# Performance work log

Hardware: AMD Instinct MI355X
Metric: run time of the kernel (lower is better)

The kernel has to match this reference:

```python
import jax, jax.numpy as jnp
import numpy as np
from math import sqrt

S, B = 512, 64
V, E, H, T = 50000, 256, 512, 9
PAD = 0

def setup_inputs() -> dict:
    key = jax.random.key(0)
    ks = jax.random.split(key, 12)
    x = jax.random.randint(ks[0], (S, B), 0, V)
    x = x.at[0].set(jnp.maximum(x[0], 1))  # first token never pad (CRF mask req)
    bio = jax.random.randint(ks[1], (S, B), 0, T)
    sc = 0.02
    return {
        "x": x, "bio": bio,
        "emb": jax.random.normal(ks[2], (V, E), jnp.float32) * sc,
        "W_ih": jax.random.normal(ks[3], (4 * H, E), jnp.float32) * sc,
        "W_hh": jax.random.normal(ks[4], (4 * H, H), jnp.float32) * sc,
        "b_ih": jnp.zeros((4 * H,), jnp.float32),
        "b_hh": jnp.zeros((4 * H,), jnp.float32),
        "W_out": jax.random.normal(ks[5], (T, H), jnp.float32) * sc,
        "b_out": jnp.zeros((T,), jnp.float32),
        "start_t": jax.random.normal(ks[6], (T,), jnp.float32) * 0.1,
        "end_t": jax.random.normal(ks[7], (T,), jnp.float32) * 0.1,
        "trans": jax.random.normal(ks[8], (T, T), jnp.float32) * 0.1,
    }

def _lstm(embeds, W_ih, W_hh, b_ih, b_hh):
    # embeds: [S,B,E] time-major, single layer, pytorch gate order i,f,g,o
    def step(carry, e_t):
        h, c = carry
        gates = e_t @ W_ih.T + h @ W_hh.T + (b_ih + b_hh)  # [B,4H]
        i, f, g, o = jnp.split(gates, 4, axis=-1)
        i, f, o = jax.nn.sigmoid(i), jax.nn.sigmoid(f), jax.nn.sigmoid(o)
        c = f * c + i * jnp.tanh(g)
        h = o * jnp.tanh(c)
        return (h, c), h
    h0 = jnp.zeros((embeds.shape[1], W_hh.shape[1]), embeds.dtype)
    _, hs = jax.lax.scan(step, (h0, h0), embeds)
    return hs  # [S,B,H]

def _crf_llh(emissions, tags, maskf, start_t, end_t, trans):
    # emissions [S,B,T], tags [S,B], maskf [S,B] float. Returns summed log-likelihood.
    Bn = emissions.shape[1]
    barange = jnp.arange(Bn)
    em = jnp.take_along_axis(emissions, tags[:, :, None], axis=2)[:, :, 0]  # [S,B]
    tr = trans[tags[:-1], tags[1:]]  # [S-1,B]
    seq_ends = maskf.sum(0).astype(jnp.int32) - 1
    last_tags = tags[seq_ends, barange]
    num = (start_t[tags[0]] + em[0]
           + ((em[1:] + tr) * maskf[1:]).sum(0)
           + end_t[last_tags])  # [B]
    # normalizer: forward algorithm
    def step(score, inp):
        e_t, m_t = inp  # [B,T], [B]
        nxt = jax.nn.logsumexp(score[:, :, None] + trans[None] + e_t[:, None, :], axis=1)
        score = jnp.where(m_t[:, None] > 0, nxt, score)
        return score, None
    score0 = start_t[None] + emissions[0]  # [B,T]
    scoreN, _ = jax.lax.scan(step, score0, (emissions[1:], maskf[1:]))
    norm = jax.nn.logsumexp(scoreN + end_t[None], axis=1)  # [B]
    return (num - norm).sum()

def _viterbi(emissions, start_t, end_t, trans):
    # full-length decode (model calls crf.decode without mask)
    Bn, Tn = emissions.shape[1], emissions.shape[2]
    barange = jnp.arange(Bn)
    def step(score, e_t):
        cand = score[:, :, None] + trans[None]  # [B,T_prev,T_next]
        idx = jnp.argmax(cand, axis=1)          # [B,T]
        score = jnp.max(cand, axis=1) + e_t
        return score, idx
    score0 = start_t[None] + emissions[0]
    scoreN, history = jax.lax.scan(step, score0, emissions[1:])  # history [S-1,B,T]
    last = jnp.argmax(scoreN + end_t[None], axis=1)  # [B]
    def back(tag, h_t):
        prev = h_t[barange, tag]
        return prev, tag
    tag0, rest = jax.lax.scan(back, last, history, reverse=True)  # rest[t] = tag_{t+1}
    return jnp.concatenate([tag0[None], rest], axis=0)  # [S,B]

def reference(x, bio, emb, W_ih, W_hh, b_ih, b_hh, W_out, b_out, start_t, end_t, trans):
    maskf = (x != PAD).astype(jnp.float32)  # [S,B]
    embeds = emb[x] * sqrt(E)               # [S,B,E]
    lstm_out = _lstm(embeds, W_ih, W_hh, b_ih, b_hh)  # [S,B,H]
    logits = lstm_out @ W_out.T + b_out               # [S,B,T]
    emissions = jax.nn.log_softmax(logits, axis=-1)
    llh = _crf_llh(emissions, bio, maskf, start_t, end_t, trans)
    crf_tags = _viterbi(emissions, start_t, end_t, trans)
    return (-llh, crf_tags)
```

## Files before the change

### kernel.cpp

```cpp
#include <hip/hip_runtime.h>
#include <math.h>

#define SS 512
#define BB 64
#define EE 256
#define HH 512
#define NT 9
#define NWG 256
#define GBG 32

#define HS_ELEMS ((size_t)SS * BB * HH)
#define EM_OFF   HS_ELEMS
#define NUM_OFF  (EM_OFF + (size_t)SS * BB * NT)
#define NORM_OFF (NUM_OFF + 64)
#define BAR_OFF  (NORM_OFF + 64)
#define BAR_U32S ((size_t)SS * 8 * 16)

#define L_WHH 0
#define L_H   32768
#define L_GSM 36928
#define L_CS  37504
#define L_TOT 37632

__global__ __launch_bounds__(256) void init_barriers(float* __restrict__ ws) {
    unsigned* bar = (unsigned*)(ws + BAR_OFF);
    size_t idx = (size_t)blockIdx.x * 256 + threadIdx.x;
    if (idx < 2 * BAR_U32S) bar[idx] = 0u;
}

__global__ __launch_bounds__(512) void lstm_persistent(
    const float* __restrict__ Whh, const float* __restrict__ Wih,
    const float* __restrict__ bih, const float* __restrict__ bhh,
    const float* __restrict__ emb, const int* __restrict__ x,
    float* __restrict__ ws)
{
    const int wg    = blockIdx.x;
    const int slice = wg & 31;
    const int bg    = wg >> 5;
    const int tid   = threadIdx.x;
    const int w     = tid >> 6;
    const int L     = tid & 63;
    const int b_l   = L & 7;
    const int kc    = L >> 3;
    const int b     = bg * 8 + b_l;

    float* hs = ws;
    unsigned* cnt  = (unsigned*)(ws + BAR_OFF);
    unsigned* flag = cnt + BAR_U32S;

    extern __shared__ float smem[];
    float* whh_l = smem + L_WHH;
    float* h_l   = smem + L_H;
    float* gsm   = smem + L_GSM;
    float* cs_l  = smem + L_CS;

    int grow[8];
#pragma unroll
    for (int r = 0; r < 8; r++) {
        int l = w * 8 + r;
        grow[r] = (l >> 4) * HH + slice * 16 + (l & 15);
    }

    for (int j = 0; j < 64; j++) {
        int idx = j * 512 + tid;
        int l = idx >> 9;
        int k = idx & 511;
        int gr = (l >> 4) * HH + slice * 16 + (l & 15);
        whh_l[idx] = Whh[(size_t)gr * HH + k];
    }

    float bs0 = 0.f, bs1 = 0.f, bs2 = 0.f, bs3 = 0.f;
    if (tid < 128) {
        const int u  = tid & 15;
        const int bb = tid >> 4;
        const int gu = slice * 16 + u;
        bs0 = bih[0 * HH + gu] + bhh[0 * HH + gu];
        bs1 = bih[1 * HH + gu] + bhh[1 * HH + gu];
        bs2 = bih[2 * HH + gu] + bhh[2 * HH + gu];
        bs3 = bih[3 * HH + gu] + bhh[3 * HH + gu];
        cs_l[u * 8 + bb] = 0.0f;
    }

#pragma unroll
    for (int j = 0; j < 8; j++) {
        int idx = j * 512 + tid;
        h_l[(idx >> 9) * 520 + (idx & 511)] = 0.0f;
    }

    float acc_ih[8];
    {
        const int xv = x[0 * BB + b];
        const float* erow = emb + (size_t)xv * EE;
#pragma unroll
        for (int r = 0; r < 8; r++) acc_ih[r] = 0.0f;
        for (int c = 0; c < 8; c++) {
            const int k0 = c * 32 + kc * 4;
            float4 e4 = *(const float4*)(erow + k0);
            e4.x *= 16.0f; e4.y *= 16.0f; e4.z *= 16.0f; e4.w *= 16.0f;
#pragma unroll
            for (int r = 0; r < 8; r++) {
                float4 w4 = *(const float4*)(Wih + (size_t)grow[r] * EE + k0);
                acc_ih[r] += w4.x * e4.x + w4.y * e4.y + w4.z * e4.z + w4.w * e4.w;
            }
        }
    }
    __syncthreads();

    const float* wbase = whh_l + (size_t)(w * 8) * 512;

    for (int t = 0; t < SS; t++) {
        float acc[8];
#pragma unroll
        for (int r = 0; r < 8; r++) acc[r] = acc_ih[r];
        const float* hrow = h_l + b_l * 520;
        for (int c = 0; c < 16; c++) {
            const int k0 = c * 32 + kc * 4;
            float4 h4 = *(const float4*)(hrow + k0);
#pragma unroll
            for (int r = 0; r < 8; r++) {
                float4 w4 = *(const float4*)(wbase + r * 512 + k0);
                acc[r] += w4.x * h4.x + w4.y * h4.y + w4.z * h4.z + w4.w * h4.w;
            }
        }

#pragma unroll
        for (int r = 0; r < 8; r++) {
            acc[r] += __shfl_xor(acc[r], 8, 64);
            acc[r] += __shfl_xor(acc[r], 16, 64);
            acc[r] += __shfl_xor(acc[r], 32, 64);
        }
        float myv = acc[0];
#pragma unroll
        for (int r = 1; r < 8; r++) if (kc == r) myv = acc[r];
        gsm[(w * 8 + kc) * 9 + b_l] = myv;
        __syncthreads();

        if (tid < 128) {
            const int u  = tid & 15;
            const int bb = tid >> 4;
            const int gu = slice * 16 + u;
            float gi = gsm[(0 * 16 + u) * 9 + bb] + bs0;
            float gf = gsm[(1 * 16 + u) * 9 + bb] + bs1;
            float gg = gsm[(2 * 16 + u) * 9 + bb] + bs2;
            float go = gsm[(3 * 16 + u) * 9 + bb] + bs3;
            float i_ = 1.0f / (1.0f + expf(-gi));
            float f_ = 1.0f / (1.0f + expf(-gf));
            float o_ = 1.0f / (1.0f + expf(-go));
            const int gb = bg * 8 + bb;
            float cn = f_ * cs_l[u * 8 + bb] + i_ * tanhf(gg);
            float hn = o_ * tanhf(cn);
            cs_l[u * 8 + bb] = cn;
            __hip_atomic_store(&hs[(size_t)t * BB * HH + (size_t)gb * HH + gu],
                               hn, __ATOMIC_RELAXED, __HIP_MEMORY_SCOPE_AGENT);
        }
        __syncthreads();

        if (tid == 0) {
            unsigned old = __hip_atomic_fetch_add(&cnt[((size_t)t * 8 + bg) * 16], 1u,
                                                  __ATOMIC_RELAXED,
                                                  __HIP_MEMORY_SCOPE_AGENT);
            if (old == GBG - 1)
                __hip_atomic_store(&flag[((size_t)t * 8 + bg) * 16], 1u,
                                   __ATOMIC_RELAXED, __HIP_MEMORY_SCOPE_AGENT);
        }

        if (t + 1 < SS) {
            {
                const int xv = x[(t + 1) * BB + b];
                const float* erow = emb + (size_t)xv * EE;
#pragma unroll
                for (int r = 0; r < 8; r++) acc_ih[r] = 0.0f;
                for (int c = 0; c < 8; c++) {
                    const int k0 = c * 32 + kc * 4;
                    float4 e4 = *(const float4*)(erow + k0);
                    e4.x *= 16.0f; e4.y *= 16.0f; e4.z *= 16.0f; e4.w *= 16.0f;
#pragma unroll
                    for (int r = 0; r < 8; r++) {
                        float4 w4 = *(const float4*)(Wih + (size_t)grow[r] * EE + k0);
                        acc_ih[r] += w4.x * e4.x + w4.y * e4.y + w4.z * e4.z + w4.w * e4.w;
                    }
                }
            }
            if (tid == 0) {
                while (__hip_atomic_load(&flag[((size_t)t * 8 + bg) * 16],
                                         __ATOMIC_RELAXED,
                                         __HIP_MEMORY_SCOPE_AGENT) == 0u) {}
            }
            __syncthreads();

            const float* hsrc = hs + (size_t)t * BB * HH + (size_t)bg * 8 * HH;
#pragma unroll
            for (int j = 0; j < 8; j++) {
                int idx = j * 512 + tid;
                float v = __hip_atomic_load(&hsrc[idx], __ATOMIC_RELAXED,
                                            __HIP_MEMORY_SCOPE_AGENT);
                h_l[(idx >> 9) * 520 + (idx & 511)] = v;
            }
            __syncthreads();
        }
    }
}

__global__ __launch_bounds__(256) void emis_kernel(
    const float* __restrict__ Wout, const float* __restrict__ bout,
    float* __restrict__ ws)
{
    int wid = blockIdx.x * 4 + (threadIdx.x >> 6);
    int L   = threadIdx.x & 63;
    const float* h = ws + (size_t)wid * HH;
    float hv[8];
#pragma unroll
    for (int i = 0; i < 8; i++) hv[i] = h[i * 64 + L];
    float acc[9];
#pragma unroll
    for (int tg = 0; tg < 9; tg++) acc[tg] = 0.0f;
    for (int i = 0; i < 8; i++) {
#pragma unroll
        for (int tg = 0; tg < 9; tg++)
            acc[tg] += Wout[tg * HH + i * 64 + L] * hv[i];
    }
#pragma unroll
    for (int tg = 0; tg < 9; tg++) {
        acc[tg] += __shfl_xor(acc[tg], 1, 64);
        acc[tg] += __shfl_xor(acc[tg], 2, 64);
        acc[tg] += __shfl_xor(acc[tg], 4, 64);
        acc[tg] += __shfl_xor(acc[tg], 8, 64);
        acc[tg] += __shfl_xor(acc[tg], 16, 64);
        acc[tg] += __shfl_xor(acc[tg], 32, 64);
    }
    float lg[9];
#pragma unroll
    for (int tg = 0; tg < 9; tg++) lg[tg] = acc[tg] + bout[tg];
    float m = lg[0];
#pragma unroll
    for (int tg = 1; tg < 9; tg++) m = fmaxf(m, lg[tg]);
    float ssum = 0.0f;
#pragma unroll
    for (int tg = 0; tg < 9; tg++) ssum += expf(lg[tg] - m);
    float lse = m + logf(ssum);
    float myo = lg[0] - lse;
#pragma unroll
    for (int tg = 1; tg < 9; tg++) if (L == tg) myo = lg[tg] - lse;
    if (L < 9) ws[EM_OFF + (size_t)wid * 9 + L] = myo;
}

__global__ __launch_bounds__(512) void crf_all(
    const int* __restrict__ x, const int* __restrict__ bio,
    const float* __restrict__ start_t, const float* __restrict__ end_t,
    const float* __restrict__ trans, float* __restrict__ ws,
    float* __restrict__ out)
{
    const float* em = ws + EM_OFF;
    const int role  = blockIdx.x >> 3;
    const int local = blockIdx.x & 7;
    const int tid   = threadIdx.x;

    __shared__ float sc[9][8];
    __shared__ unsigned char hist[SS - 1][8][9];

    if (role == 0) {
        int b = local * 8 + (tid >> 6);
        int L = tid & 63;
        float sum = 0.0f;
        int cntm = 0;
#pragma unroll
        for (int j = 0; j < 8; j++) {
            int s = j * 64 + L;
            int tg = bio[s * BB + b];
            bool mk = (x[s * BB + b] != 0);
            cntm += mk ? 1 : 0;
            if (s == 0) {
                sum += start_t[tg] + em[(size_t)b * 9 + tg];
            } else if (mk) {
                int tp = bio[(s - 1) * BB + b];
                sum += em[((size_t)s * BB + b) * 9 + tg] + trans[tp * 9 + tg];
            }
        }
#pragma unroll
        for (int d = 1; d < 64; d <<= 1) {
            sum += __shfl_xor(sum, d, 64);
            cntm += __shfl_xor(cntm, d, 64);
        }
        if (L == 0) {
            int se = cntm - 1;
            sum += end_t[bio[se * BB + b]];
            ws[NUM_OFF + b] = sum;
        }
        return;
    }

    const int b_l = tid & 7;
    const int j   = tid >> 3;
    const int b   = local * 8 + b_l;
    float tc[9];
    if (j < 9) {
#pragma unroll
        for (int i = 0; i < 9; i++) tc[i] = trans[i * 9 + j];
        sc[j][b_l] = start_t[j] + em[(size_t)b * 9 + j];
    }
    __syncthreads();

    if (role == 1) {
        for (int s = 1; s < SS; s++) {
            float nv = 0.0f;
            if (j < 9) {
                float sv[9];
                float m = -3.4e38f;
#pragma unroll
                for (int i = 0; i < 9; i++) {
                    sv[i] = sc[i][b_l] + tc[i];
                    m = fmaxf(m, sv[i]);
                }
                float ssum = 0.0f;
#pragma unroll
                for (int i = 0; i < 9; i++) ssum += expf(sv[i] - m);
                nv = m + logf(ssum) + em[((size_t)s * BB + b) * 9 + j];
            }
            bool mk = (x[s * BB + b] != 0);
            __syncthreads();
            if (j < 9 && mk) sc[j][b_l] = nv;
            __syncthreads();
        }
        if (j == 0) {
            float m = -3.4e38f;
#pragma unroll
            for (int i = 0; i < 9; i++) m = fmaxf(m, sc[i][b_l] + end_t[i]);
            float ssum = 0.0f;
#pragma unroll
            for (int i = 0; i < 9; i++) ssum += expf(sc[i][b_l] + end_t[i] - m);
            ws[NORM_OFF + b] = m + logf(ssum);
        }
    } else {
        for (int s = 1; s < SS; s++) {
            float nv = 0.0f;
            if (j < 9) {
                float best = sc[0][b_l] + tc[0];
                int bi = 0;
#pragma unroll
                for (int i = 1; i < 9; i++) {
                    float v = sc[i][b_l] + tc[i];
                    if (v > best) { best = v; bi = i; }
                }
                hist[s - 1][b_l][j] = (unsigned char)bi;
                nv = best + em[((size_t)s * BB + b) * 9 + j];
            }
            __syncthreads();
            if (j < 9) sc[j][b_l] = nv;
            __syncthreads();
        }
        if (tid < 8) {
            int bl = tid;
            int gb = local * 8 + bl;
            float best = sc[0][bl] + end_t[0];
            int cur = 0;
#pragma unroll
            for (int i = 1; i < 9; i++) {
                float v = sc[i][bl] + end_t[i];
                if (v > best) { best = v; cur = i; }
            }
            out[1 + (size_t)(SS - 1) * BB + gb] = (float)cur;
            for (int s = SS - 2; s >= 0; s--) {
                cur = hist[s][bl][cur];
                out[1 + (size_t)s * BB + gb] = (float)cur;
            }
        }
    }
}

__global__ __launch_bounds__(64) void final_llh(const float* __restrict__ ws,
                                               float* __restrict__ out)
{
    int L = threadIdx.x;
    float v = ws[NUM_OFF + L] - ws[NORM_OFF + L];
    v += __shfl_xor(v, 1, 64);
    v += __shfl_xor(v, 2, 64);
    v += __shfl_xor(v, 4, 64);
    v += __shfl_xor(v, 8, 64);
    v += __shfl_xor(v, 16, 64);
    v += __shfl_xor(v, 32, 64);
    if (L == 0) out[0] = -v;
}

extern "C" void kernel_launch(void* const* d_in, const int* in_sizes, int n_in,
                              void* d_out, int out_size, void* d_ws, size_t ws_size,
                              hipStream_t stream) {
    const int*   x       = (const int*)d_in[0];
    const int*   bio     = (const int*)d_in[1];
    const float* emb     = (const float*)d_in[2];
    const float* W_ih    = (const float*)d_in[3];
    const float* W_hh    = (const float*)d_in[4];
    const float* b_ih    = (const float*)d_in[5];
    const float* b_hh    = (const float*)d_in[6];
    const float* W_out   = (const float*)d_in[7];
    const float* b_out   = (const float*)d_in[8];
    const float* start_t = (const float*)d_in[9];
    const float* end_t   = (const float*)d_in[10];
    const float* trans   = (const float*)d_in[11];
    float* out = (float*)d_out;
    float* ws  = (float*)d_ws;

    const size_t dyn_lds = (size_t)L_TOT * sizeof(float);
    static bool attr_set = false;
    if (!attr_set) {
        hipFuncSetAttribute((const void*)lstm_persistent,
                            hipFuncAttributeMaxDynamicSharedMemorySize,
                            (int)dyn_lds);
        attr_set = true;
    }

    init_barriers<<<512, 256, 0, stream>>>(ws);
    lstm_persistent<<<NWG, 512, dyn_lds, stream>>>(W_hh, W_ih, b_ih, b_hh, emb, x, ws);
    emis_kernel<<<SS * BB / 4, 256, 0, stream>>>(W_out, b_out, ws);
    crf_all<<<24, 512, 0, stream>>>(x, bio, start_t, end_t, trans, ws, out);
    final_llh<<<1, 64, 0, stream>>>(ws, out);
}
```

Measured before the change: 6.099 ms.

## Repartition LSTM recurrence across workgroups and replace counter barrier with per-WG flags

The persistent LSTM kernel now splits work into 64 hidden-row groups × 4 batch groups of 16, in place of 32 slices × 8 batch groups of 8. Each workgroup holds half as many W_hh rows in LDS and reuses each weight load across two batch halves. The atomic-counter-plus-flag barrier is replaced by per-workgroup flags that a whole wavefront polls with __all, removing the serialized fetch_add. Hidden states are written in a new packed layout, and the emissions kernel is updated to match. The trade-off is a wider group of 64 producers to wait on per batch group and a scattered LDS gather of h.

```diff
diff --git a/kernel.cpp b/kernel.cpp
--- a/kernel.cpp
+++ b/kernel.cpp
@@ -7,25 +7,24 @@
 #define HH 512
 #define NT 9
 #define NWG 256
-#define GBG 32
-
-#define HS_ELEMS ((size_t)SS * BB * HH)
-#define EM_OFF   HS_ELEMS
+
+#define HP_ELEMS ((size_t)SS * 4 * 64 * 128)
+#define EM_OFF   HP_ELEMS
 #define NUM_OFF  (EM_OFF + (size_t)SS * BB * NT)
 #define NORM_OFF (NUM_OFF + 64)
-#define BAR_OFF  (NORM_OFF + 64)
-#define BAR_U32S ((size_t)SS * 8 * 16)
+#define FLAG_OFF (NORM_OFF + 64)
+#define FLAG_U32S ((size_t)SS * 4 * 64)
 
 #define L_WHH 0
-#define L_H   32768
-#define L_GSM 36928
-#define L_CS  37504
-#define L_TOT 37632
-
-__global__ __launch_bounds__(256) void init_barriers(float* __restrict__ ws) {
-    unsigned* bar = (unsigned*)(ws + BAR_OFF);
+#define L_HL  16384
+#define L_GSM 24704
+#define L_CS  25248
+#define L_TOT 25376
+
+__global__ __launch_bounds__(256) void init_flags(float* __restrict__ ws) {
+    unsigned* f = (unsigned*)(ws + FLAG_OFF);
     size_t idx = (size_t)blockIdx.x * 256 + threadIdx.x;
-    if (idx < 2 * BAR_U32S) bar[idx] = 0u;
+    if (idx < FLAG_U32S) f[idx] = 0u;
 }
 
 __global__ __launch_bounds__(512) void lstm_persistent(
@@ -34,167 +33,172 @@
     const float* __restrict__ emb, const int* __restrict__ x,
     float* __restrict__ ws)
 {
-    const int wg    = blockIdx.x;
-    const int slice = wg & 31;
-    const int bg    = wg >> 5;
-    const int tid   = threadIdx.x;
-    const int w     = tid >> 6;
-    const int L     = tid & 63;
-    const int b_l   = L & 7;
-    const int kc    = L >> 3;
-    const int b     = bg * 8 + b_l;
-
-    float* hs = ws;
-    unsigned* cnt  = (unsigned*)(ws + BAR_OFF);
-    unsigned* flag = cnt + BAR_U32S;
+    const int wg  = blockIdx.x;
+    const int rg  = wg & 63;
+    const int bgr = wg >> 6;
+    const int tid = threadIdx.x;
+    const int w   = tid >> 6;
+    const int L   = tid & 63;
+    const int b_l = L & 7;
+    const int kc  = L >> 3;
+
+    float* hp = ws;
+    unsigned* flags = (unsigned*)(ws + FLAG_OFF);
 
     extern __shared__ float smem[];
     float* whh_l = smem + L_WHH;
-    float* h_l   = smem + L_H;
+    float* h_l   = smem + L_HL;
     float* gsm   = smem + L_GSM;
     float* cs_l  = smem + L_CS;
 
-    int grow[8];
-#pragma unroll
-    for (int r = 0; r < 8; r++) {
-        int l = w * 8 + r;
-        grow[r] = (l >> 4) * HH + slice * 16 + (l & 15);
-    }
-
-    for (int j = 0; j < 64; j++) {
-        int idx = j * 512 + tid;
-        int l = idx >> 9;
-        int k = idx & 511;
-        int gr = (l >> 4) * HH + slice * 16 + (l & 15);
+    for (int i = 0; i < 32; i++) {
+        int idx = i * 512 + tid;
+        int l = idx >> 9, k = idx & 511;
+        int gr = (l >> 3) * HH + rg * 8 + (l & 7);
         whh_l[idx] = Whh[(size_t)gr * HH + k];
     }
 
     float bs0 = 0.f, bs1 = 0.f, bs2 = 0.f, bs3 = 0.f;
     if (tid < 128) {
-        const int u  = tid & 15;
-        const int bb = tid >> 4;
-        const int gu = slice * 16 + u;
+        const int u  = tid & 7;
+        const int bb = tid >> 3;
+        const int gu = rg * 8 + u;
         bs0 = bih[0 * HH + gu] + bhh[0 * HH + gu];
         bs1 = bih[1 * HH + gu] + bhh[1 * HH + gu];
         bs2 = bih[2 * HH + gu] + bhh[2 * HH + gu];
         bs3 = bih[3 * HH + gu] + bhh[3 * HH + gu];
-        cs_l[u * 8 + bb] = 0.0f;
-    }
-
-#pragma unroll
-    for (int j = 0; j < 8; j++) {
-        int idx = j * 512 + tid;
-        h_l[(idx >> 9) * 520 + (idx & 511)] = 0.0f;
+        cs_l[u * 16 + bb] = 0.0f;
+    }
+
+    for (int i = 0; i < 17; i++) {
+        int idx = i * 512 + tid;
+        if (idx < 8320) h_l[idx] = 0.0f;
+    }
+
+    int grow[4];
+#pragma unroll
+    for (int r = 0; r < 4; r++) {
+        int l = w * 4 + r;
+        grow[r] = (l >> 3) * HH + rg * 8 + (l & 7);
     }
 
     float acc_ih[8];
-    {
-        const int xv = x[0 * BB + b];
+#pragma unroll
+    for (int i = 0; i < 8; i++) acc_ih[i] = 0.0f;
+#pragma unroll
+    for (int bh = 0; bh < 2; bh++) {
+        int xv = x[0 * BB + bgr * 16 + bh * 8 + b_l];
         const float* erow = emb + (size_t)xv * EE;
-#pragma unroll
-        for (int r = 0; r < 8; r++) acc_ih[r] = 0.0f;
         for (int c = 0; c < 8; c++) {
             const int k0 = c * 32 + kc * 4;
             float4 e4 = *(const float4*)(erow + k0);
             e4.x *= 16.0f; e4.y *= 16.0f; e4.z *= 16.0f; e4.w *= 16.0f;
 #pragma unroll
-            for (int r = 0; r < 8; r++) {
+            for (int r = 0; r < 4; r++) {
                 float4 w4 = *(const float4*)(Wih + (size_t)grow[r] * EE + k0);
-                acc_ih[r] += w4.x * e4.x + w4.y * e4.y + w4.z * e4.z + w4.w * e4.w;
+                acc_ih[r * 2 + bh] += w4.x * e4.x + w4.y * e4.y +
+                                      w4.z * e4.z + w4.w * e4.w;
             }
         }
     }
     __syncthreads();
 
-    const float* wbase = whh_l + (size_t)(w * 8) * 512;
+    const float* wbase = whh_l + (size_t)(w * 4) * 512;
 
     for (int t = 0; t < SS; t++) {
         float acc[8];
 #pragma unroll
-        for (int r = 0; r < 8; r++) acc[r] = acc_ih[r];
-        const float* hrow = h_l + b_l * 520;
+        for (int i = 0; i < 8; i++) acc[i] = acc_ih[i];
+        const float* hra = h_l + b_l * 520;
+        const float* hrb = h_l + 4160 + b_l * 520;
         for (int c = 0; c < 16; c++) {
             const int k0 = c * 32 + kc * 4;
-            float4 h4 = *(const float4*)(hrow + k0);
-#pragma unroll
-            for (int r = 0; r < 8; r++) {
+            float4 ha = *(const float4*)(hra + k0);
+            float4 hb = *(const float4*)(hrb + k0);
+#pragma unroll
+            for (int r = 0; r < 4; r++) {
                 float4 w4 = *(const float4*)(wbase + r * 512 + k0);
-                acc[r] += w4.x * h4.x + w4.y * h4.y + w4.z * h4.z + w4.w * h4.w;
-            }
-        }
-
-#pragma unroll
-        for (int r = 0; r < 8; r++) {
-            acc[r] += __shfl_xor(acc[r], 8, 64);
-            acc[r] += __shfl_xor(acc[r], 16, 64);
-            acc[r] += __shfl_xor(acc[r], 32, 64);
+                acc[r * 2 + 0] += w4.x * ha.x + w4.y * ha.y +
+                                  w4.z * ha.z + w4.w * ha.w;
+                acc[r * 2 + 1] += w4.x * hb.x + w4.y * hb.y +
+                                  w4.z * hb.z + w4.w * hb.w;
+            }
+        }
+
+#pragma unroll
+        for (int i = 0; i < 8; i++) {
+            acc[i] += __shfl_xor(acc[i], 8, 64);
+            acc[i] += __shfl_xor(acc[i], 16, 64);
+            acc[i] += __shfl_xor(acc[i], 32, 64);
         }
         float myv = acc[0];
 #pragma unroll
-        for (int r = 1; r < 8; r++) if (kc == r) myv = acc[r];
-        gsm[(w * 8 + kc) * 9 + b_l] = myv;
+        for (int j = 1; j < 8; j++)
+            if (kc == j) myv = acc[(j & 3) * 2 + (j >> 2)];
+        gsm[(w * 4 + (kc & 3)) * 17 + (kc >> 2) * 8 + b_l] = myv;
         __syncthreads();
 
         if (tid < 128) {
-            const int u  = tid & 15;
-            const int bb = tid >> 4;
-            const int gu = slice * 16 + u;
-            float gi = gsm[(0 * 16 + u) * 9 + bb] + bs0;
-            float gf = gsm[(1 * 16 + u) * 9 + bb] + bs1;
-            float gg = gsm[(2 * 16 + u) * 9 + bb] + bs2;
-            float go = gsm[(3 * 16 + u) * 9 + bb] + bs3;
-            float i_ = 1.0f / (1.0f + expf(-gi));
-            float f_ = 1.0f / (1.0f + expf(-gf));
-            float o_ = 1.0f / (1.0f + expf(-go));
-            const int gb = bg * 8 + bb;
-            float cn = f_ * cs_l[u * 8 + bb] + i_ * tanhf(gg);
+            const int u  = tid & 7;
+            const int bb = tid >> 3;
+            float g0 = gsm[(0 * 8 + u) * 17 + bb] + bs0;
+            float g1 = gsm[(1 * 8 + u) * 17 + bb] + bs1;
+            float g2 = gsm[(2 * 8 + u) * 17 + bb] + bs2;
+            float g3 = gsm[(3 * 8 + u) * 17 + bb] + bs3;
+            float i_ = 1.0f / (1.0f + expf(-g0));
+            float f_ = 1.0f / (1.0f + expf(-g1));
+            float o_ = 1.0f / (1.0f + expf(-g3));
+            float cn = f_ * cs_l[u * 16 + bb] + i_ * tanhf(g2);
             float hn = o_ * tanhf(cn);
-            cs_l[u * 8 + bb] = cn;
-            __hip_atomic_store(&hs[(size_t)t * BB * HH + (size_t)gb * HH + gu],
-                               hn, __ATOMIC_RELAXED, __HIP_MEMORY_SCOPE_AGENT);
+            cs_l[u * 16 + bb] = cn;
+            __hip_atomic_store(
+                &hp[(((size_t)t * 4 + bgr) * 64 + rg) * 128 + tid],
+                hn, __ATOMIC_RELAXED, __HIP_MEMORY_SCOPE_AGENT);
         }
         __syncthreads();
 
-        if (tid == 0) {
-            unsigned old = __hip_atomic_fetch_add(&cnt[((size_t)t * 8 + bg) * 16], 1u,
-                                                  __ATOMIC_RELAXED,
-                                                  __HIP_MEMORY_SCOPE_AGENT);
-            if (old == GBG - 1)
-                __hip_atomic_store(&flag[((size_t)t * 8 + bg) * 16], 1u,
+        if (t + 1 < SS) {
+            if (tid == 0)
+                __hip_atomic_store(&flags[((size_t)t * 4 + bgr) * 64 + rg], 1u,
                                    __ATOMIC_RELAXED, __HIP_MEMORY_SCOPE_AGENT);
-        }
-
-        if (t + 1 < SS) {
-            {
-                const int xv = x[(t + 1) * BB + b];
+
+#pragma unroll
+            for (int i = 0; i < 8; i++) acc_ih[i] = 0.0f;
+#pragma unroll
+            for (int bh = 0; bh < 2; bh++) {
+                int xv = x[(t + 1) * BB + bgr * 16 + bh * 8 + b_l];
                 const float* erow = emb + (size_t)xv * EE;
-#pragma unroll
-                for (int r = 0; r < 8; r++) acc_ih[r] = 0.0f;
                 for (int c = 0; c < 8; c++) {
                     const int k0 = c * 32 + kc * 4;
                     float4 e4 = *(const float4*)(erow + k0);
                     e4.x *= 16.0f; e4.y *= 16.0f; e4.z *= 16.0f; e4.w *= 16.0f;
 #pragma unroll
-                    for (int r = 0; r < 8; r++) {
+                    for (int r = 0; r < 4; r++) {
                         float4 w4 = *(const float4*)(Wih + (size_t)grow[r] * EE + k0);
-                        acc_ih[r] += w4.x * e4.x + w4.y * e4.y + w4.z * e4.z + w4.w * e4.w;
+                        acc_ih[r * 2 + bh] += w4.x * e4.x + w4.y * e4.y +
+                                              w4.z * e4.z + w4.w * e4.w;
                     }
                 }
             }
-            if (tid == 0) {
-                while (__hip_atomic_load(&flag[((size_t)t * 8 + bg) * 16],
-                                         __ATOMIC_RELAXED,
-                                         __HIP_MEMORY_SCOPE_AGENT) == 0u) {}
-            }
-            __syncthreads();
-
-            const float* hsrc = hs + (size_t)t * BB * HH + (size_t)bg * 8 * HH;
-#pragma unroll
-            for (int j = 0; j < 8; j++) {
-                int idx = j * 512 + tid;
+
+            if (w == 0) {
+                const unsigned* fl = flags + ((size_t)t * 4 + bgr) * 64;
+                for (;;) {
+                    unsigned v = __hip_atomic_load(&fl[L], __ATOMIC_RELAXED,
+                                                   __HIP_MEMORY_SCOPE_AGENT);
+                    if (__all(v != 0u)) break;
+                }
+            }
+            __syncthreads();
+
+            const float* hsrc = hp + ((size_t)t * 4 + bgr) * 64 * 128;
+#pragma unroll
+            for (int i = 0; i < 16; i++) {
+                int idx = i * 512 + tid;
                 float v = __hip_atomic_load(&hsrc[idx], __ATOMIC_RELAXED,
                                             __HIP_MEMORY_SCOPE_AGENT);
-                h_l[(idx >> 9) * 520 + (idx & 511)] = v;
+                int bb = (idx >> 3) & 15, u = idx & 7, rg2 = idx >> 7;
+                h_l[(bb >> 3) * 4160 + (bb & 7) * 520 + rg2 * 8 + u] = v;
             }
             __syncthreads();
         }
@@ -207,10 +211,12 @@
 {
     int wid = blockIdx.x * 4 + (threadIdx.x >> 6);
     int L   = threadIdx.x & 63;
-    const float* h = ws + (size_t)wid * HH;
+    int t = wid >> 6, b = wid & 63;
+    const float* hb = ws + ((size_t)t * 4 + (b >> 4)) * 64 * 128;
     float hv[8];
 #pragma unroll
-    for (int i = 0; i < 8; i++) hv[i] = h[i * 64 + L];
+    for (int i = 0; i < 8; i++)
+        hv[i] = hb[(size_t)(i * 8 + (L >> 3)) * 128 + (b & 15) * 8 + (L & 7)];
     float acc[9];
 #pragma unroll
     for (int tg = 0; tg < 9; tg++) acc[tg] = 0.0f;
@@ -400,15 +406,11 @@
     float* ws  = (float*)d_ws;
 
     const size_t dyn_lds = (size_t)L_TOT * sizeof(float);
-    static bool attr_set = false;
-    if (!attr_set) {
-        hipFuncSetAttribute((const void*)lstm_persistent,
-                            hipFuncAttributeMaxDynamicSharedMemorySize,
-                            (int)dyn_lds);
-        attr_set = true;
-    }
-
-    init_barriers<<<512, 256, 0, stream>>>(ws);
+    hipFuncSetAttribute((const void*)lstm_persistent,
+                        hipFuncAttributeMaxDynamicSharedMemorySize,
+                        (int)dyn_lds);
+
+    init_flags<<<512, 256, 0, stream>>>(ws);
     lstm_persistent<<<NWG, 512, dyn_lds, stream>>>(W_hh, W_ih, b_ih, b_hh, emb, x, ws);
     emis_kernel<<<SS * BB / 4, 256, 0, stream>>>(W_out, b_out, ws);
     crf_all<<<24, 512, 0, stream>>>(x, bio, start_t, end_t, trans, ws, out);
```

Measured after the change: 11.62 ms. 90.4% more time.
